# Optimization experiments

Hardware: AMD Instinct MI355X
Metric: run time of the kernel (lower is better)

Reference implementation:

```python
import jax, jax.numpy as jnp
import numpy as np

N_POINTS, N_TYPES, PER_TYPE, HIST, IN_U, U = 32768, 4, 8192, 32, 128, 128

def setup_inputs() -> dict:
    key = jax.random.key(0)
    ks = jax.random.split(key, 8)
    return {
        "current_node_state": jax.random.normal(ks[0], (N_POINTS, IN_U), jnp.float32),
        "historical_buffer": jax.random.normal(ks[1], (N_POINTS, HIST, U), jnp.float32),
        "entity_idx": jax.random.randint(ks[2], (N_TYPES, PER_TYPE), 0, N_POINTS, jnp.int32),
        "q_w": jax.random.normal(ks[3], (N_TYPES, IN_U, U), jnp.float32),
        "k_w": jax.random.normal(ks[4], (N_TYPES, U, U), jnp.float32),
        "v_w": jax.random.normal(ks[5], (N_TYPES, U, U), jnp.float32),
        "fc_w": jax.random.normal(ks[6], (N_TYPES, U, U), jnp.float32),
    }

def reference(current_node_state, historical_buffer, entity_idx, q_w, k_w, v_w, fc_w):
    # Batched-by-type gather (the original Python loop over entity types,
    # vectorized since all types have equal counts here).
    x = current_node_state[entity_idx]        # (T, N, IN_U)
    h = historical_buffer[entity_idx]         # (T, N, H, U)
    q = jnp.einsum('tne,teu->tnu', x, q_w)[:, :, None, :]   # (T, N, 1, U)
    k = jnp.einsum('tnhu,tuv->tnhv', h, k_w)                # (T, N, H, U)
    v = jnp.einsum('tnhu,tuv->tnhv', h, v_w)                # (T, N, H, U)
    raw = jnp.einsum('tnou,tnhu->tnoh', q, k)               # (T, N, 1, H)
    # NOTE: original uses F.softmax(raw_score) with implicit dim; for a 3D
    # tensor torch's legacy rule picks dim=0 (the per-type entity axis).
    attn = jax.nn.softmax(raw, axis=1)                      # softmax over N within each type
    agg = jnp.einsum('tnoh,tnhu->tnou', attn, v)            # (T, N, 1, U)
    out = jax.nn.relu(jnp.einsum('tnou,tuv->tnov', agg, fc_w)) + q
    # cat over types along node dim, then final squeeze -> (n_points, U)
    return out.reshape(N_TYPES * PER_TYPE, U)
```

## Files before the change

### kernel.cpp

```cpp
#include <hip/hip_runtime.h>
#include <math.h>

#define NPTS 32768
#define NTYPES 4
#define PER_TYPE 8192
#define HIST 32
#define UD 128
#define XT_STRIDE 68


__device__ __forceinline__ unsigned fkey(float x) {
    unsigned b = __float_as_uint(x);
    return (b & 0x80000000u) ? ~b : (b | 0x80000000u);
}
__device__ __forceinline__ float funkey(unsigned k) {
    unsigned b = (k & 0x80000000u) ? (k & 0x7fffffffu) : ~k;
    return __uint_as_float(b);
}

__global__ __launch_bounds__(128) void prep_kernel(
    const float* __restrict__ k_w, const float* __restrict__ v_w,
    const float* __restrict__ fc_w, float* __restrict__ kT,
    float* __restrict__ wvf, unsigned* __restrict__ Mbits, float* __restrict__ S)
{
    int r = blockIdx.x;
    int t = blockIdx.y;
    int u = threadIdx.x;
    kT[(t * UD + r) * UD + u] = k_w[(t * UD + u) * UD + r];
    float acc = 0.f;
    const float* vrow = v_w + (t * UD + r) * UD;
    const float* fb = fc_w + t * UD * UD;
    #pragma unroll 8
    for (int m = 0; m < UD; ++m)
        acc = fmaf(vrow[m], fb[m * UD + u], acc);
    wvf[(t * UD + r) * UD + u] = acc;
    if (r == 0 && t == 0) { Mbits[u] = 0u; S[u] = 0.f; }
}

__global__ __launch_bounds__(256) void qqk_kernel(
    const float* __restrict__ x, const int* __restrict__ idx,
    const float* __restrict__ q_w, const float* __restrict__ kT,
    float* __restrict__ q_out, float* __restrict__ qk_out)
{
    __shared__ float xT[UD * XT_STRIDE];
    __shared__ float qT[UD * XT_STRIDE];
    __shared__ int srow[64];
    int tx = threadIdx.x;
    int bn = blockIdx.x;
    int t  = blockIdx.y;
    int n0 = bn * 64;

    if (tx < 64) srow[tx] = idx[t * PER_TYPE + n0 + tx];
    __syncthreads();

    {
        int e = tx & 127;
        int half = tx >> 7;
        for (int i = 0; i < 32; ++i) {
            int ent = half * 32 + i;
            xT[e * XT_STRIDE + ent] = x[(size_t)srow[ent] * UD + e];
        }
    }
    __syncthreads();

    const int c4 = (tx & 31) * 4;
    const int eg = tx >> 5;
    float acc[8][4];

    #pragma unroll
    for (int i = 0; i < 8; ++i)
        #pragma unroll
        for (int j = 0; j < 4; ++j) acc[i][j] = 0.f;
    {
        const float* qw = q_w + t * UD * UD;
        for (int e = 0; e < UD; ++e) {
            float4 w = *(const float4*)(qw + e * UD + c4);
            const float* xr = &xT[e * XT_STRIDE + eg * 8];
            float4 a0 = *(const float4*)(xr);
            float4 a1 = *(const float4*)(xr + 4);
            float av[8] = {a0.x, a0.y, a0.z, a0.w, a1.x, a1.y, a1.z, a1.w};
            #pragma unroll
            for (int i = 0; i < 8; ++i) {
                acc[i][0] = fmaf(av[i], w.x, acc[i][0]);
                acc[i][1] = fmaf(av[i], w.y, acc[i][1]);
                acc[i][2] = fmaf(av[i], w.z, acc[i][2]);
                acc[i][3] = fmaf(av[i], w.w, acc[i][3]);
            }
        }
    }
    #pragma unroll
    for (int i = 0; i < 8; ++i) {
        int g = t * PER_TYPE + n0 + eg * 8 + i;
        *(float4*)(q_out + (size_t)g * UD + c4) =
            make_float4(acc[i][0], acc[i][1], acc[i][2], acc[i][3]);
    }
    #pragma unroll
    for (int j = 0; j < 4; ++j) {
        float4 lo = make_float4(acc[0][j], acc[1][j], acc[2][j], acc[3][j]);
        float4 hi = make_float4(acc[4][j], acc[5][j], acc[6][j], acc[7][j]);
        *(float4*)(&qT[(c4 + j) * XT_STRIDE + eg * 8]) = lo;
        *(float4*)(&qT[(c4 + j) * XT_STRIDE + eg * 8 + 4]) = hi;
    }
    __syncthreads();

    #pragma unroll
    for (int i = 0; i < 8; ++i)
        #pragma unroll
        for (int j = 0; j < 4; ++j) acc[i][j] = 0.f;
    {
        const float* kw = kT + t * UD * UD;
        for (int v = 0; v < UD; ++v) {
            float4 w = *(const float4*)(kw + v * UD + c4);
            const float* qr = &qT[v * XT_STRIDE + eg * 8];
            float4 a0 = *(const float4*)(qr);
            float4 a1 = *(const float4*)(qr + 4);
            float av[8] = {a0.x, a0.y, a0.z, a0.w, a1.x, a1.y, a1.z, a1.w};
            #pragma unroll
            for (int i = 0; i < 8; ++i) {
                acc[i][0] = fmaf(av[i], w.x, acc[i][0]);
                acc[i][1] = fmaf(av[i], w.y, acc[i][1]);
                acc[i][2] = fmaf(av[i], w.z, acc[i][2]);
                acc[i][3] = fmaf(av[i], w.w, acc[i][3]);
            }
        }
    }
    #pragma unroll
    for (int i = 0; i < 8; ++i) {
        int g = t * PER_TYPE + n0 + eg * 8 + i;
        *(float4*)(qk_out + (size_t)g * UD + c4) =
            make_float4(acc[i][0], acc[i][1], acc[i][2], acc[i][3]);
    }
}

__global__ __launch_bounds__(256) void raw_kernel(
    const float* __restrict__ hist, const int* __restrict__ idx,
    const float* __restrict__ qk, float* __restrict__ raw,
    unsigned* __restrict__ Mbits)
{
    __shared__ int srow[16];
    __shared__ float sqk[16 * UD];
    __shared__ unsigned smax[HIST];
    int tx = threadIdx.x;
    int bn = blockIdx.x;
    int t  = blockIdx.y;
    int n0 = bn * 16;
    if (tx < 16) srow[tx] = idx[t * PER_TYPE + n0 + tx];
    if (tx < HIST) smax[tx] = 0u;
    {
        int e = tx >> 4;
        int c = (tx & 15) * 8;
        const float* src = qk + ((size_t)(t * PER_TYPE + n0 + e)) * UD + c;
        float4 a = *(const float4*)(src);
        float4 b = *(const float4*)(src + 4);
        *(float4*)(&sqk[e * UD + c]) = a;
        *(float4*)(&sqk[e * UD + c + 4]) = b;
    }
    __syncthreads();

    int sub = tx & 3;
    int hh  = (tx >> 2) & 31;
    int eh  = tx >> 7;
    float vmax = -INFINITY;
    for (int j = 0; j < 8; ++j) {
        int ei = j * 2 + eh;
        int g  = t * PER_TYPE + n0 + ei;
        const float* hr = hist + ((size_t)srow[ei] * HIST + hh) * UD + sub * 32;
        float4 h0 = *(const float4*)(hr);
        float4 h1 = *(const float4*)(hr + 4);
        float4 h2 = *(const float4*)(hr + 8);
        float4 h3 = *(const float4*)(hr + 12);
        float4 h4 = *(const float4*)(hr + 16);
        float4 h5 = *(const float4*)(hr + 20);
        float4 h6 = *(const float4*)(hr + 24);
        float4 h7 = *(const float4*)(hr + 28);
        const float* qr = &sqk[ei * UD + sub * 32];
        float4 q0 = *(const float4*)(qr);
        float4 q1 = *(const float4*)(qr + 4);
        float4 q2 = *(const float4*)(qr + 8);
        float4 q3 = *(const float4*)(qr + 12);
        float4 q4 = *(const float4*)(qr + 16);
        float4 q5 = *(const float4*)(qr + 20);
        float4 q6 = *(const float4*)(qr + 24);
        float4 q7 = *(const float4*)(qr + 28);
        float p0 = q0.x * h0.x + q0.y * h0.y + q0.z * h0.z + q0.w * h0.w;
        float p1 = q1.x * h1.x + q1.y * h1.y + q1.z * h1.z + q1.w * h1.w;
        float p2 = q2.x * h2.x + q2.y * h2.y + q2.z * h2.z + q2.w * h2.w;
        float p3 = q3.x * h3.x + q3.y * h3.y + q3.z * h3.z + q3.w * h3.w;
        p0 = fmaf(q4.x, h4.x, fmaf(q4.y, h4.y, fmaf(q4.z, h4.z, fmaf(q4.w, h4.w, p0))));
        p1 = fmaf(q5.x, h5.x, fmaf(q5.y, h5.y, fmaf(q5.z, h5.z, fmaf(q5.w, h5.w, p1))));
        p2 = fmaf(q6.x, h6.x, fmaf(q6.y, h6.y, fmaf(q6.z, h6.z, fmaf(q6.w, h6.w, p2))));
        p3 = fmaf(q7.x, h7.x, fmaf(q7.y, h7.y, fmaf(q7.z, h7.z, fmaf(q7.w, h7.w, p3))));
        float a = (p0 + p1) + (p2 + p3);
        a += __shfl_xor(a, 1);
        a += __shfl_xor(a, 2);
        vmax = fmaxf(vmax, a);
        if (sub == 0) raw[(size_t)g * HIST + hh] = a;
    }
    if (sub == 0) atomicMax(&smax[hh], fkey(vmax));
    __syncthreads();
    if (tx < HIST) atomicMax(&Mbits[t * HIST + tx], smax[tx]);
}

__global__ __launch_bounds__(256) void sum_kernel(
    const float* __restrict__ raw, const unsigned* __restrict__ Mbits,
    float* __restrict__ S)
{
    __shared__ float red[8][32];
    int tx = threadIdx.x;
    int c = blockIdx.x;
    int t = blockIdx.y;
    int hh = tx & 31;
    int nsl = tx >> 5;
    float M = funkey(Mbits[t * HIST + hh]);
    float s = 0.f;
    for (int i = 0; i < 32; ++i) {
        int n = c * 256 + i * 8 + nsl;
        float r = raw[((size_t)t * PER_TYPE + n) * HIST + hh];
        float e = r - M;
        if (e > -85.f) s += expf(e);
    }
    red[nsl][hh] = s;
    __syncthreads();
    if (tx < 32) {
        float tot = 0.f;
        #pragma unroll
        for (int k = 0; k < 8; ++k) tot += red[k][tx];
        atomicAdd(&S[t * HIST + tx], tot);
    }
}

__global__ __launch_bounds__(256) void out_kernel(
    const float* __restrict__ hist, const int* __restrict__ idx,
    const float* __restrict__ q, const float* __restrict__ raw,
    const unsigned* __restrict__ Mbits, const float* __restrict__ S,
    const float* __restrict__ wvf, float* __restrict__ out)
{
    __shared__ float shbar[4][UD];
    int tx = threadIdx.x;
    int wave = tx >> 6;
    int lane = tx & 63;
    int g = blockIdx.x * 4 + wave;
    int t = g >> 13;
    float w = 0.f;
    if (lane < 32) {
        float r = raw[(size_t)g * HIST + lane];
        float M = funkey(Mbits[t * HIST + lane]);
        float e = r - M;
        if (e > -75.f) w = expf(e) / S[t * HIST + lane];
    }
    unsigned long long act = __ballot(w != 0.f);
    int u2 = lane * 2;
    float2 qv = *(const float2*)(q + (size_t)g * UD + u2);
    float2 o;
    if (act == 0ull) {
        o = qv;
    } else {
        int row = idx[g];
        float2 hb = make_float2(0.f, 0.f);
        unsigned long long m = act;
        while (m) {
            int hh = __ffsll(m) - 1;
            m &= m - 1;
            float wv = __shfl(w, hh);
            float2 hv = *(const float2*)(hist + ((size_t)row * HIST + hh) * UD + u2);
            hb.x = fmaf(wv, hv.x, hb.x);
            hb.y = fmaf(wv, hv.y, hb.y);
        }
        shbar[wave][u2] = hb.x;
        shbar[wave][u2 + 1] = hb.y;
        float2 a = make_float2(0.f, 0.f);
        const float* wt = wvf + t * UD * UD;
        for (int e = 0; e < UD; ++e) {
            float hbe = shbar[wave][e];
            float2 wr = *(const float2*)(wt + e * UD + u2);
            a.x = fmaf(hbe, wr.x, a.x);
            a.y = fmaf(hbe, wr.y, a.y);
        }
        o.x = fmaxf(a.x, 0.f) + qv.x;
        o.y = fmaxf(a.y, 0.f) + qv.y;
    }
    *(float2*)(out + (size_t)g * UD + u2) = o;
}

extern "C" void kernel_launch(void* const* d_in, const int* in_sizes, int n_in,
                              void* d_out, int out_size, void* d_ws, size_t ws_size,
                              hipStream_t stream) {
    const float* x    = (const float*)d_in[0];
    const float* hist = (const float*)d_in[1];
    const int*   idx  = (const int*)d_in[2];
    const float* q_w  = (const float*)d_in[3];
    const float* k_w  = (const float*)d_in[4];
    const float* v_w  = (const float*)d_in[5];
    const float* fc_w = (const float*)d_in[6];
    float* out = (float*)d_out;

    float* ws = (float*)d_ws;
    float* q     = ws;
    float* qk    = ws + 4194304;
    float* raw   = ws + 8388608;
    unsigned* Mb = (unsigned*)(ws + 9437184);
    float* S     = ws + 9437312;
    float* kT    = ws + 9437440;
    float* wvf   = ws + 9502976;

    prep_kernel<<<dim3(128, 4), 128, 0, stream>>>(k_w, v_w, fc_w, kT, wvf, Mb, S);
    qqk_kernel<<<dim3(128, 4), 256, 0, stream>>>(x, idx, q_w, kT, q, qk);
    raw_kernel<<<dim3(512, 4), 256, 0, stream>>>(hist, idx, qk, raw, Mb);
    sum_kernel<<<dim3(32, 4), 256, 0, stream>>>(raw, Mb, S);
    out_kernel<<<8192, 256, 0, stream>>>(hist, idx, q, raw, Mb, S, wvf, out);
}
```

Before: 750.8 us.

## Use online softmax partials with merge kernel and halve qqk tile size

Replaces the global atomicMax over keyed floats plus a separate sum pass over raw scores with an online (max, sum) computation inside raw_kernel. Each block writes its partial max and sum, and a small merge kernel combines them per (type, hist) column. This removes the second full read of the raw buffer and the atomics. Separately, qqk_kernel now handles 32 entities per block instead of 64, doubling the grid and shrinking shared memory and registers. The cost is more repeated weight loads per entity and some extra exp work in raw_kernel.

Measured after the change: 747.9 us (median of 2 runs). No clear change (-0.4%).

```diff
diff --git a/kernel.cpp b/kernel.cpp
--- a/kernel.cpp
+++ b/kernel.cpp
@@ -6,22 +6,13 @@
 #define PER_TYPE 8192
 #define HIST 32
 #define UD 128
-#define XT_STRIDE 68
-
-
-__device__ __forceinline__ unsigned fkey(float x) {
-    unsigned b = __float_as_uint(x);
-    return (b & 0x80000000u) ? ~b : (b | 0x80000000u);
-}
-__device__ __forceinline__ float funkey(unsigned k) {
-    unsigned b = (k & 0x80000000u) ? (k & 0x7fffffffu) : ~k;
-    return __uint_as_float(b);
-}
+#define XT_STRIDE 36
+
 
 __global__ __launch_bounds__(128) void prep_kernel(
     const float* __restrict__ k_w, const float* __restrict__ v_w,
     const float* __restrict__ fc_w, float* __restrict__ kT,
-    float* __restrict__ wvf, unsigned* __restrict__ Mbits, float* __restrict__ S)
+    float* __restrict__ wvf)
 {
     int r = blockIdx.x;
     int t = blockIdx.y;
@@ -34,7 +25,6 @@
     for (int m = 0; m < UD; ++m)
         acc = fmaf(vrow[m], fb[m * UD + u], acc);
     wvf[(t * UD + r) * UD + u] = acc;
-    if (r == 0 && t == 0) { Mbits[u] = 0u; S[u] = 0.f; }
 }
 
 __global__ __launch_bounds__(256) void qqk_kernel(
@@ -44,20 +34,20 @@
 {
     __shared__ float xT[UD * XT_STRIDE];
     __shared__ float qT[UD * XT_STRIDE];
-    __shared__ int srow[64];
+    __shared__ int srow[32];
     int tx = threadIdx.x;
     int bn = blockIdx.x;
     int t  = blockIdx.y;
-    int n0 = bn * 64;
-
-    if (tx < 64) srow[tx] = idx[t * PER_TYPE + n0 + tx];
+    int n0 = bn * 32;
+
+    if (tx < 32) srow[tx] = idx[t * PER_TYPE + n0 + tx];
     __syncthreads();
 
     {
         int e = tx & 127;
         int half = tx >> 7;
-        for (int i = 0; i < 32; ++i) {
-            int ent = half * 32 + i;
+        for (int i = 0; i < 16; ++i) {
+            int ent = half * 16 + i;
             xT[e * XT_STRIDE + ent] = x[(size_t)srow[ent] * UD + e];
         }
     }
@@ -65,22 +55,20 @@
 
     const int c4 = (tx & 31) * 4;
     const int eg = tx >> 5;
-    float acc[8][4];
-
-    #pragma unroll
-    for (int i = 0; i < 8; ++i)
+    float acc[4][4];
+
+    #pragma unroll
+    for (int i = 0; i < 4; ++i)
         #pragma unroll
         for (int j = 0; j < 4; ++j) acc[i][j] = 0.f;
     {
         const float* qw = q_w + t * UD * UD;
         for (int e = 0; e < UD; ++e) {
             float4 w = *(const float4*)(qw + e * UD + c4);
-            const float* xr = &xT[e * XT_STRIDE + eg * 8];
-            float4 a0 = *(const float4*)(xr);
-            float4 a1 = *(const float4*)(xr + 4);
-            float av[8] = {a0.x, a0.y, a0.z, a0.w, a1.x, a1.y, a1.z, a1.w};
+            float4 a0 = *(const float4*)(&xT[e * XT_STRIDE + eg * 4]);
+            float av[4] = {a0.x, a0.y, a0.z, a0.w};
             #pragma unroll
-            for (int i = 0; i < 8; ++i) {
+            for (int i = 0; i < 4; ++i) {
                 acc[i][0] = fmaf(av[i], w.x, acc[i][0]);
                 acc[i][1] = fmaf(av[i], w.y, acc[i][1]);
                 acc[i][2] = fmaf(av[i], w.z, acc[i][2]);
@@ -89,34 +77,30 @@
         }
     }
     #pragma unroll
-    for (int i = 0; i < 8; ++i) {
-        int g = t * PER_TYPE + n0 + eg * 8 + i;
+    for (int i = 0; i < 4; ++i) {
+        int g = t * PER_TYPE + n0 + eg * 4 + i;
         *(float4*)(q_out + (size_t)g * UD + c4) =
             make_float4(acc[i][0], acc[i][1], acc[i][2], acc[i][3]);
     }
     #pragma unroll
     for (int j = 0; j < 4; ++j) {
-        float4 lo = make_float4(acc[0][j], acc[1][j], acc[2][j], acc[3][j]);
-        float4 hi = make_float4(acc[4][j], acc[5][j], acc[6][j], acc[7][j]);
-        *(float4*)(&qT[(c4 + j) * XT_STRIDE + eg * 8]) = lo;
-        *(float4*)(&qT[(c4 + j) * XT_STRIDE + eg * 8 + 4]) = hi;
-    }
-    __syncthreads();
-
-    #pragma unroll
-    for (int i = 0; i < 8; ++i)
+        *(float4*)(&qT[(c4 + j) * XT_STRIDE + eg * 4]) =
+            make_float4(acc[0][j], acc[1][j], acc[2][j], acc[3][j]);
+    }
+    __syncthreads();
+
+    #pragma unroll
+    for (int i = 0; i < 4; ++i)
         #pragma unroll
         for (int j = 0; j < 4; ++j) acc[i][j] = 0.f;
     {
         const float* kw = kT + t * UD * UD;
         for (int v = 0; v < UD; ++v) {
             float4 w = *(const float4*)(kw + v * UD + c4);
-            const float* qr = &qT[v * XT_STRIDE + eg * 8];
-            float4 a0 = *(const float4*)(qr);
-            float4 a1 = *(const float4*)(qr + 4);
-            float av[8] = {a0.x, a0.y, a0.z, a0.w, a1.x, a1.y, a1.z, a1.w};
+            float4 a0 = *(const float4*)(&qT[v * XT_STRIDE + eg * 4]);
+            float av[4] = {a0.x, a0.y, a0.z, a0.w};
             #pragma unroll
-            for (int i = 0; i < 8; ++i) {
+            for (int i = 0; i < 4; ++i) {
                 acc[i][0] = fmaf(av[i], w.x, acc[i][0]);
                 acc[i][1] = fmaf(av[i], w.y, acc[i][1]);
                 acc[i][2] = fmaf(av[i], w.z, acc[i][2]);
@@ -125,8 +109,8 @@
         }
     }
     #pragma unroll
-    for (int i = 0; i < 8; ++i) {
-        int g = t * PER_TYPE + n0 + eg * 8 + i;
+    for (int i = 0; i < 4; ++i) {
+        int g = t * PER_TYPE + n0 + eg * 4 + i;
         *(float4*)(qk_out + (size_t)g * UD + c4) =
             make_float4(acc[i][0], acc[i][1], acc[i][2], acc[i][3]);
     }
@@ -135,17 +119,17 @@
 __global__ __launch_bounds__(256) void raw_kernel(
     const float* __restrict__ hist, const int* __restrict__ idx,
     const float* __restrict__ qk, float* __restrict__ raw,
-    unsigned* __restrict__ Mbits)
+    float* __restrict__ pm, float* __restrict__ ps)
 {
     __shared__ int srow[16];
     __shared__ float sqk[16 * UD];
-    __shared__ unsigned smax[HIST];
+    __shared__ float sm[HIST][2];
+    __shared__ float ss[HIST][2];
     int tx = threadIdx.x;
     int bn = blockIdx.x;
     int t  = blockIdx.y;
     int n0 = bn * 16;
     if (tx < 16) srow[tx] = idx[t * PER_TYPE + n0 + tx];
-    if (tx < HIST) smax[tx] = 0u;
     {
         int e = tx >> 4;
         int c = (tx & 15) * 8;
@@ -160,7 +144,7 @@
     int sub = tx & 3;
     int hh  = (tx >> 2) & 31;
     int eh  = tx >> 7;
-    float vmax = -INFINITY;
+    float m = -INFINITY, s = 0.f;
     for (int j = 0; j < 8; ++j) {
         int ei = j * 2 + eh;
         int g  = t * PER_TYPE + n0 + ei;
@@ -193,46 +177,63 @@
         float a = (p0 + p1) + (p2 + p3);
         a += __shfl_xor(a, 1);
         a += __shfl_xor(a, 2);
-        vmax = fmaxf(vmax, a);
         if (sub == 0) raw[(size_t)g * HIST + hh] = a;
-    }
-    if (sub == 0) atomicMax(&smax[hh], fkey(vmax));
-    __syncthreads();
-    if (tx < HIST) atomicMax(&Mbits[t * HIST + tx], smax[tx]);
-}
-
-__global__ __launch_bounds__(256) void sum_kernel(
-    const float* __restrict__ raw, const unsigned* __restrict__ Mbits,
-    float* __restrict__ S)
-{
-    __shared__ float red[8][32];
+        float mo = m;
+        m = fmaxf(m, a);
+        s = s * __expf(mo - m) + __expf(a - m);
+    }
+    if (sub == 0) { sm[hh][eh] = m; ss[hh][eh] = s; }
+    __syncthreads();
+    if (tx < HIST) {
+        float m0 = sm[tx][0], m1 = sm[tx][1];
+        float M = fmaxf(m0, m1);
+        float S = ss[tx][0] * __expf(m0 - M) + ss[tx][1] * __expf(m1 - M);
+        pm[((size_t)t * HIST + tx) * 512 + bn] = M;
+        ps[((size_t)t * HIST + tx) * 512 + bn] = S;
+    }
+}
+
+__global__ __launch_bounds__(256) void merge_kernel(
+    const float* __restrict__ pm, const float* __restrict__ ps,
+    float* __restrict__ Mf, float* __restrict__ S)
+{
+    int b = blockIdx.x;
     int tx = threadIdx.x;
-    int c = blockIdx.x;
-    int t = blockIdx.y;
-    int hh = tx & 31;
-    int nsl = tx >> 5;
-    float M = funkey(Mbits[t * HIST + hh]);
-    float s = 0.f;
-    for (int i = 0; i < 32; ++i) {
-        int n = c * 256 + i * 8 + nsl;
-        float r = raw[((size_t)t * PER_TYPE + n) * HIST + hh];
-        float e = r - M;
-        if (e > -85.f) s += expf(e);
-    }
-    red[nsl][hh] = s;
-    __syncthreads();
-    if (tx < 32) {
-        float tot = 0.f;
-        #pragma unroll
-        for (int k = 0; k < 8; ++k) tot += red[k][tx];
-        atomicAdd(&S[t * HIST + tx], tot);
+    float m = -INFINITY, s = 0.f;
+    #pragma unroll
+    for (int i = 0; i < 2; ++i) {
+        int k = tx + i * 256;
+        float pmv = pm[(size_t)b * 512 + k];
+        float psv = ps[(size_t)b * 512 + k];
+        float M = fmaxf(m, pmv);
+        s = s * expf(m - M) + psv * expf(pmv - M);
+        m = M;
+    }
+    #pragma unroll
+    for (int off = 1; off < 64; off <<= 1) {
+        float om = __shfl_xor(m, off);
+        float os = __shfl_xor(s, off);
+        float M = fmaxf(m, om);
+        s = s * expf(m - M) + os * expf(om - M);
+        m = M;
+    }
+    __shared__ float rm[4], rs[4];
+    int wave = tx >> 6, lane = tx & 63;
+    if (lane == 0) { rm[wave] = m; rs[wave] = s; }
+    __syncthreads();
+    if (tx == 0) {
+        float M = fmaxf(fmaxf(rm[0], rm[1]), fmaxf(rm[2], rm[3]));
+        float Sv = rs[0] * expf(rm[0] - M) + rs[1] * expf(rm[1] - M)
+                 + rs[2] * expf(rm[2] - M) + rs[3] * expf(rm[3] - M);
+        Mf[b] = M;
+        S[b] = Sv;
     }
 }
 
 __global__ __launch_bounds__(256) void out_kernel(
     const float* __restrict__ hist, const int* __restrict__ idx,
     const float* __restrict__ q, const float* __restrict__ raw,
-    const unsigned* __restrict__ Mbits, const float* __restrict__ S,
+    const float* __restrict__ Mf, const float* __restrict__ S,
     const float* __restrict__ wvf, float* __restrict__ out)
 {
     __shared__ float shbar[4][UD];
@@ -244,7 +245,7 @@
     float w = 0.f;
     if (lane < 32) {
         float r = raw[(size_t)g * HIST + lane];
-        float M = funkey(Mbits[t * HIST + lane]);
+        float M = Mf[t * HIST + lane];
         float e = r - M;
         if (e > -75.f) w = expf(e) / S[t * HIST + lane];
     }
@@ -298,14 +299,16 @@
     float* q     = ws;
     float* qk    = ws + 4194304;
     float* raw   = ws + 8388608;
-    unsigned* Mb = (unsigned*)(ws + 9437184);
+    float* Mf    = ws + 9437184;
     float* S     = ws + 9437312;
     float* kT    = ws + 9437440;
     float* wvf   = ws + 9502976;
-
-    prep_kernel<<<dim3(128, 4), 128, 0, stream>>>(k_w, v_w, fc_w, kT, wvf, Mb, S);
-    qqk_kernel<<<dim3(128, 4), 256, 0, stream>>>(x, idx, q_w, kT, q, qk);
-    raw_kernel<<<dim3(512, 4), 256, 0, stream>>>(hist, idx, qk, raw, Mb);
-    sum_kernel<<<dim3(32, 4), 256, 0, stream>>>(raw, Mb, S);
-    out_kernel<<<8192, 256, 0, stream>>>(hist, idx, q, raw, Mb, S, wvf, out);
-}
+    float* pm    = ws + 9568512;
+    float* ps    = ws + 9634048;
+
+    prep_kernel<<<dim3(128, 4), 128, 0, stream>>>(k_w, v_w, fc_w, kT, wvf);
+    qqk_kernel<<<dim3(256, 4), 256, 0, stream>>>(x, idx, q_w, kT, q, qk);
+    raw_kernel<<<dim3(512, 4), 256, 0, stream>>>(hist, idx, qk, raw, pm, ps);
+    merge_kernel<<<128, 256, 0, stream>>>(pm, ps, Mf, S);
+    out_kernel<<<8192, 256, 0, stream>>>(hist, idx, q, raw, Mf, S, wvf, out);
+}
```
